# Optimization experiments

Hardware: AMD Instinct MI355X
Metric: run time of the kernel (lower is better)

## Reference

```python
import jax, jax.numpy as jnp
import numpy as np

QUERY_SIZE = 128


def setup_inputs() -> dict:
    key = jax.random.key(0)
    ks = jax.random.split(key, 4)
    S, B, T, E, Q = 512, 32, 1024, 512, QUERY_SIZE
    query = jax.random.normal(ks[0], (S, B, Q), dtype=jnp.float32)
    embedded_text = jax.random.normal(ks[1], (T, B, E), dtype=jnp.float32)
    text_mask = jnp.ones((T, B), dtype=jnp.float32)
    position = jnp.zeros((S, B), dtype=jnp.float32)
    # nn.Linear(query_size, 2): W [2, Q], b [2]; kaiming-uniform-ish init scale
    lim = 1.0 / np.sqrt(Q)
    W = jax.random.uniform(ks[2], (2, Q), dtype=jnp.float32, minval=-lim, maxval=lim)
    b = jax.random.uniform(ks[3], (2,), dtype=jnp.float32, minval=-lim, maxval=lim)
    return {"query": query, "embedded_text": embedded_text, "text_mask": text_mask,
            "position": position, "W": W, "b": b}


def reference(query, embedded_text, text_mask, position, W, b):
    # query: [S,B,Q], embedded_text: [T,B,E], text_mask: [T,B], position: [S,B]
    masked_embedding = embedded_text * text_mask[:, :, None]          # [T,B,E]
    query_result = jnp.exp(query @ W.T + b)                           # [S,B,2]
    mean_raw = query_result[..., 0]                                   # [S,B]
    std = query_result[..., 1]                                        # [S,B]
    mean = position + jnp.cumsum(mean_raw, axis=0) / 20.0             # [S,B]
    T = embedded_text.shape[0]
    indices = jnp.arange(T, dtype=query.dtype)                        # [T]
    # Gaussian window weights over text positions: [S,T,B]
    weights = jnp.exp(-std[:, None, :] * (mean[:, None, :] - indices[None, :, None]) ** 2)
    # Reduce over text_len without materializing [S,T,B,E]
    new_context = jnp.einsum('stb,tbe->sbe', weights, masked_embedding)  # [S,B,E]
    return new_context, mean
```

## Files before the change

kernel.cpp:

```cpp
#include <hip/hip_runtime.h>
#include <hip/hip_bf16.h>


#define S_DIM 512
#define B_DIM 32
#define T_DIM 1024
#define E_DIM 512
#define Q_DIM 128
#define WIN_CUT 20.0f
#define CH 16
#define TSEG 64

__global__ __launch_bounds__(256) void dot_kernel(
    const float* __restrict__ query,
    const float* __restrict__ W,
    const float* __restrict__ bias,
    float* __restrict__ ws_mraw,
    float* __restrict__ ws_std)
{
    const int wave = threadIdx.x >> 6;
    const int lane = threadIdx.x & 63;
    const int pair = blockIdx.x * 4 + wave;
    const float2* qp = (const float2*)(query + (size_t)pair * Q_DIM);
    float2 v = qp[lane];
    float d0 = v.x * W[2 * lane]         + v.y * W[2 * lane + 1];
    float d1 = v.x * W[Q_DIM + 2 * lane] + v.y * W[Q_DIM + 2 * lane + 1];
    #pragma unroll
    for (int off = 32; off; off >>= 1) {
        d0 += __shfl_down(d0, off);
        d1 += __shfl_down(d1, off);
    }
    if (lane == 0) {
        int s = pair / B_DIM, b = pair % B_DIM;
        ws_mraw[(size_t)b * S_DIM + s] = expf(d0 + bias[0]);
        ws_std[(size_t)b * S_DIM + s]  = expf(d1 + bias[1]);
    }
}

__global__ __launch_bounds__(64) void scan_kernel(
    const float* __restrict__ ws_mraw,
    const float* __restrict__ position,
    float* __restrict__ ws_mean,
    float* __restrict__ out_mean)
{
    const int b = blockIdx.x;
    const int lane = threadIdx.x;
    const float4* src = (const float4*)(ws_mraw + (size_t)b * S_DIM + lane * 8);
    float4 x0 = src[0], x1 = src[1];
    float v[8] = {x0.x, x0.y, x0.z, x0.w, x1.x, x1.y, x1.z, x1.w};
    float pre[8], run = 0.f;
    #pragma unroll
    for (int j = 0; j < 8; ++j) { run += v[j]; pre[j] = run; }
    float tot = run, sc = tot;
    #pragma unroll
    for (int off = 1; off < 64; off <<= 1) {
        float u = __shfl_up(sc, off);
        if (lane >= off) sc += u;
    }
    float excl = sc - tot;
    #pragma unroll
    for (int j = 0; j < 8; ++j) {
        int s = lane * 8 + j;
        float m = position[(size_t)s * B_DIM + b] + (excl + pre[j]) * 0.05f;
        ws_mean[(size_t)b * S_DIM + s] = m;
        out_mean[(size_t)s * B_DIM + b] = m;
    }
}

__global__ __launch_bounds__(128) void ctx_kernel(
    const float* __restrict__ emb,
    const float* __restrict__ mask,
    const float* __restrict__ ws_mean,
    const float* __restrict__ ws_std,
    float* __restrict__ out)
{
    __shared__ float lds_w[TSEG * CH];
    __shared__ float lds_mean[CH], lds_std[CH];
    __shared__ int s_tlo, s_thi;
    const int c = blockIdx.x, b = blockIdx.y;
    const int s0 = c * CH;
    const int tid = threadIdx.x;

    if (tid < CH) {
        lds_mean[tid] = ws_mean[(size_t)b * S_DIM + s0 + tid];
        lds_std[tid]  = ws_std[(size_t)b * S_DIM + s0 + tid];
    }
    __syncthreads();
    if (tid == 0) {
        float lo = 1e30f, hi = -1e30f;
        #pragma unroll
        for (int i = 0; i < CH; ++i) {
            float r = __fsqrt_rn(WIN_CUT / lds_std[i]);
            lo = fminf(lo, lds_mean[i] - r);
            hi = fmaxf(hi, lds_mean[i] + r);
        }
        int tlo = (int)floorf(lo);
        if (tlo < 0) tlo = 0; if (tlo > T_DIM - 1) tlo = T_DIM - 1;
        int thi = (int)ceilf(hi);
        if (thi > T_DIM - 1) thi = T_DIM - 1; if (thi < tlo) thi = tlo;
        s_tlo = tlo; s_thi = thi;
    }
    __syncthreads();
    const int tlo = s_tlo, thi = s_thi;

    float4 acc[CH];
    #pragma unroll
    for (int i = 0; i < CH; ++i) acc[i] = float4{0.f, 0.f, 0.f, 0.f};

    for (int tseg = tlo; tseg <= thi; tseg += TSEG) {
        {
            const int toff = tid >> 1;
            const int ibase = (tid & 1) * 8;
            const int t = tseg + toff;
            float mv = 0.f;
            if (t <= thi) mv = mask[(size_t)t * B_DIM + b];
            #pragma unroll
            for (int j = 0; j < 8; ++j) {
                int i = ibase + j;
                float d = lds_mean[i] - (float)t;
                float w = (t <= thi) ? __expf(-lds_std[i] * d * d) * mv : 0.f;
                lds_w[toff * CH + i] = w;
            }
        }
        __syncthreads();
        const int tend = (thi < tseg + TSEG - 1) ? thi : (tseg + TSEG - 1);
        for (int t = tseg; t <= tend; ++t) {
            const int toff = t - tseg;
            const float4 v =
                ((const float4*)(emb + ((size_t)t * B_DIM + b) * E_DIM))[tid];
            const float* wrow = lds_w + toff * CH;
            #pragma unroll
            for (int i = 0; i < CH; ++i) {
                float w = wrow[i];
                acc[i].x += w * v.x; acc[i].y += w * v.y;
                acc[i].z += w * v.z; acc[i].w += w * v.w;
            }
        }
        __syncthreads();
    }
    #pragma unroll
    for (int i = 0; i < CH; ++i)
        ((float4*)(out + ((size_t)(s0 + i) * B_DIM + b) * E_DIM))[tid] = acc[i];
}

extern "C" void kernel_launch(void* const* d_in, const int* in_sizes, int n_in,
                              void* d_out, int out_size, void* d_ws, size_t ws_size,
                              hipStream_t stream) {
    const float* query = (const float*)d_in[0];
    const float* emb   = (const float*)d_in[1];
    const float* mask  = (const float*)d_in[2];
    const float* pos   = (const float*)d_in[3];
    const float* W     = (const float*)d_in[4];
    const float* bias  = (const float*)d_in[5];

    float* out_ctx  = (float*)d_out;
    float* out_mean = out_ctx + (size_t)S_DIM * B_DIM * E_DIM;

    float* ws_mraw = (float*)d_ws;
    float* ws_std  = ws_mraw + (size_t)S_DIM * B_DIM;
    float* ws_mean = ws_std  + (size_t)S_DIM * B_DIM;

    dot_kernel<<<(S_DIM * B_DIM) / 4, 256, 0, stream>>>(query, W, bias, ws_mraw, ws_std);
    scan_kernel<<<B_DIM, 64, 0, stream>>>(ws_mraw, pos, ws_mean, out_mean);
    ctx_kernel<<<dim3(S_DIM / CH, B_DIM), 128, 0, stream>>>(emb, mask, ws_mean, ws_std, out_ctx);
}
```

Baseline: 130.8 us.

## Split ctx_kernel query chunk across two thread halves with prefetch and nontemporal stores

Doubles the ctx block to 256 threads, with each half accumulating 8 of the 16 query rows, so each thread holds half as many accumulators and each block has twice as many waves to hide latency. The embedding row for the next text position is loaded one iteration ahead, weights are written to LDS as vectors, window bounds are computed in parallel, and outputs use nontemporal stores. In exchange, each embedding row is now loaded by both halves, roughly doubling L1/L2 traffic for emb.

```diff
diff --git a/kernel.cpp b/kernel.cpp
--- a/kernel.cpp
+++ b/kernel.cpp
@@ -10,6 +10,8 @@
 #define WIN_CUT 20.0f
 #define CH 16
 #define TSEG 64
+
+typedef float v4f __attribute__((ext_vector_type(4)));
 
 __global__ __launch_bounds__(256) void dot_kernel(
     const float* __restrict__ query,
@@ -67,7 +69,7 @@
     }
 }
 
-__global__ __launch_bounds__(128) void ctx_kernel(
+__global__ __launch_bounds__(256) void ctx_kernel(
     const float* __restrict__ emb,
     const float* __restrict__ mask,
     const float* __restrict__ ws_mean,
@@ -76,23 +78,30 @@
 {
     __shared__ float lds_w[TSEG * CH];
     __shared__ float lds_mean[CH], lds_std[CH];
+    __shared__ float lds_lo[CH], lds_hi[CH];
     __shared__ int s_tlo, s_thi;
     const int c = blockIdx.x, b = blockIdx.y;
     const int s0 = c * CH;
     const int tid = threadIdx.x;
+    const int half = tid >> 7;
+    const int htid = tid & 127;
 
     if (tid < CH) {
-        lds_mean[tid] = ws_mean[(size_t)b * S_DIM + s0 + tid];
-        lds_std[tid]  = ws_std[(size_t)b * S_DIM + s0 + tid];
+        float m  = ws_mean[(size_t)b * S_DIM + s0 + tid];
+        float sd = ws_std[(size_t)b * S_DIM + s0 + tid];
+        lds_mean[tid] = m;
+        lds_std[tid]  = sd;
+        float r = __fsqrt_rn(WIN_CUT / sd);
+        lds_lo[tid] = m - r;
+        lds_hi[tid] = m + r;
     }
     __syncthreads();
     if (tid == 0) {
         float lo = 1e30f, hi = -1e30f;
         #pragma unroll
         for (int i = 0; i < CH; ++i) {
-            float r = __fsqrt_rn(WIN_CUT / lds_std[i]);
-            lo = fminf(lo, lds_mean[i] - r);
-            hi = fmaxf(hi, lds_mean[i] + r);
+            lo = fminf(lo, lds_lo[i]);
+            hi = fmaxf(hi, lds_hi[i]);
         }
         int tlo = (int)floorf(lo);
         if (tlo < 0) tlo = 0; if (tlo > T_DIM - 1) tlo = T_DIM - 1;
@@ -103,44 +112,48 @@
     __syncthreads();
     const int tlo = s_tlo, thi = s_thi;
 
-    float4 acc[CH];
+    v4f acc[8];
     #pragma unroll
-    for (int i = 0; i < CH; ++i) acc[i] = float4{0.f, 0.f, 0.f, 0.f};
+    for (int i = 0; i < 8; ++i) acc[i] = (v4f)0.f;
 
     for (int tseg = tlo; tseg <= thi; tseg += TSEG) {
         {
-            const int toff = tid >> 1;
-            const int ibase = (tid & 1) * 8;
+            const int toff = tid >> 2;
+            const int ibase = (tid & 3) * 4;
             const int t = tseg + toff;
             float mv = 0.f;
             if (t <= thi) mv = mask[(size_t)t * B_DIM + b];
+            v4f w;
             #pragma unroll
-            for (int j = 0; j < 8; ++j) {
+            for (int j = 0; j < 4; ++j) {
                 int i = ibase + j;
                 float d = lds_mean[i] - (float)t;
-                float w = (t <= thi) ? __expf(-lds_std[i] * d * d) * mv : 0.f;
-                lds_w[toff * CH + i] = w;
+                w[j] = (t <= thi) ? __expf(-lds_std[i] * d * d) * mv : 0.f;
             }
+            *(v4f*)(lds_w + toff * CH + ibase) = w;
         }
         __syncthreads();
         const int tend = (thi < tseg + TSEG - 1) ? thi : (tseg + TSEG - 1);
+        const float* wbase = lds_w + half * 8;
+        v4f v = ((const v4f*)(emb + ((size_t)tseg * B_DIM + b) * E_DIM))[htid];
         for (int t = tseg; t <= tend; ++t) {
-            const int toff = t - tseg;
-            const float4 v =
-                ((const float4*)(emb + ((size_t)t * B_DIM + b) * E_DIM))[tid];
-            const float* wrow = lds_w + toff * CH;
+            const int tn = (t < tend) ? t + 1 : t;
+            v4f vn = ((const v4f*)(emb + ((size_t)tn * B_DIM + b) * E_DIM))[htid];
+            const float* wrow = wbase + (t - tseg) * CH;
             #pragma unroll
-            for (int i = 0; i < CH; ++i) {
+            for (int i = 0; i < 8; ++i) {
                 float w = wrow[i];
-                acc[i].x += w * v.x; acc[i].y += w * v.y;
-                acc[i].z += w * v.z; acc[i].w += w * v.w;
+                acc[i] += w * v;
             }
+            v = vn;
         }
         __syncthreads();
     }
     #pragma unroll
-    for (int i = 0; i < CH; ++i)
-        ((float4*)(out + ((size_t)(s0 + i) * B_DIM + b) * E_DIM))[tid] = acc[i];
+    for (int i = 0; i < 8; ++i) {
+        v4f* dst = (v4f*)(out + ((size_t)(s0 + half * 8 + i) * B_DIM + b) * E_DIM);
+        __builtin_nontemporal_store(acc[i], dst + htid);
+    }
 }
 
 extern "C" void kernel_launch(void* const* d_in, const int* in_sizes, int n_in,
@@ -162,5 +175,5 @@
 
     dot_kernel<<<(S_DIM * B_DIM) / 4, 256, 0, stream>>>(query, W, bias, ws_mraw, ws_std);
     scan_kernel<<<B_DIM, 64, 0, stream>>>(ws_mraw, pos, ws_mean, out_mean);
-    ctx_kernel<<<dim3(S_DIM / CH, B_DIM), 128, 0, stream>>>(emb, mask, ws_mean, ws_std, out_ctx);
+    ctx_kernel<<<dim3(S_DIM / CH, B_DIM), 256, 0, stream>>>(emb, mask, ws_mean, ws_std, out_ctx);
 }
```

Result: no change. 129.3 us (-1.1%).
